# Kernel optimization log

Measured on AMD Instinct MI355X. Metric: run time of the kernel, lower is better.

Reference implementation:

```python
import jax, jax.numpy as jnp
import numpy as np

DEG_CLAMP = 1e6  # matches .clamp(max=1000000.0) on deg^-0.5


def setup_inputs() -> dict:
    key = jax.random.key(0)
    k1, k2, k3 = jax.random.split(key, 3)
    N, E, D_IN, D_OUT = 100000, 1600000, 128, 128
    x = jax.random.normal(k1, (N, D_IN), dtype=jnp.float32)
    edge_index = jax.random.randint(k2, (2, E), 0, N, dtype=jnp.int64)
    # Linear params (xavier_uniform on weight, zero-ish bias)
    limit = float(np.sqrt(6.0 / (D_IN + D_OUT)))
    W = jax.random.uniform(k3, (D_OUT, D_IN), dtype=jnp.float32, minval=-limit, maxval=limit)
    b = jnp.zeros((D_OUT,), dtype=jnp.float32)
    return {"x": x, "edge_index": edge_index, "W": W, "b": b}


def reference(x, edge_index, W, b):
    N = x.shape[0]
    # append self-loops: ei = cat([edge_index, [arange(N); arange(N)]], dim=1)
    self_idx = jnp.arange(N, dtype=edge_index.dtype)
    src = jnp.concatenate([edge_index[0], self_idx])  # [E+N]
    dst = jnp.concatenate([edge_index[1], self_idx])  # [E+N]
    # degree of destination nodes (with self-loops)
    deg = jax.ops.segment_sum(jnp.ones_like(dst, dtype=x.dtype), dst, num_segments=N)
    deg_inv_sqrt = jnp.minimum(deg ** -0.5, DEG_CLAMP)
    # linear transform (dropout is identity in eval)
    h = x @ W.T + b  # [N, D_OUT]
    # symmetric normalization, gather, scale, scatter-add
    norm = deg_inv_sqrt[src] * deg_inv_sqrt[dst]  # [E+N]
    msgs = h[src] * norm[:, None]                  # [E+N, D_OUT]
    out = jax.ops.segment_sum(msgs, dst, num_segments=N)  # [N, D_OUT]
    return out
```

## Files before the change

kernel.cpp:

```cpp
#include <hip/hip_runtime.h>
#include <hip/hip_bf16.h>
#include <cstddef>

#define D 128
#define SHIFT 9
#define RN (1 << SHIFT)
#define CAPLOG 14
#define CAP (1 << CAPLOG)

typedef __attribute__((ext_vector_type(8))) short bf16x8;
typedef __attribute__((ext_vector_type(16))) float f32x16;
typedef __attribute__((ext_vector_type(4))) float f32x4;

static __device__ __forceinline__ unsigned short f2bf(float f) {
  return __builtin_bit_cast(unsigned short, __float2bfloat16(f));
}
static __device__ __forceinline__ float bflo(unsigned u) {
  return __uint_as_float(u << 16);
}
static __device__ __forceinline__ float bfhi(unsigned u) {
  return __uint_as_float(u & 0xffff0000u);
}

__global__ void k_init(int* __restrict__ gcursor, int nc, unsigned* __restrict__ gz,
                       const float* __restrict__ W, unsigned short* __restrict__ Wbf) {
  const int t = blockIdx.x * 256 + threadIdx.x;
  if (t < nc) gcursor[t] = t << CAPLOG;
  if (t < 64) gz[t] = 0;
  if (t < 128 * 128) Wbf[t] = f2bf(W[t]);
}

__global__ __launch_bounds__(256) void k_psort(
    const int* __restrict__ src, const int* __restrict__ dst,
    int* __restrict__ gcursor, unsigned* __restrict__ pairs, int e, int nc) {
  __shared__ int hist4[4][256];
  const int tid = threadIdx.x;
  const int w = tid >> 6;
  const int base = blockIdx.x * 4096;
  const int m = min(4096, e - base);
#pragma unroll
  for (int u = 0; u < 4; ++u) ((int*)hist4)[tid + 256 * u] = 0;
  __syncthreads();
  int myd[16], mys[16];
#pragma unroll
  for (int j = 0; j < 16; ++j) {
    const int i = tid + j * 256;
    if (i < m) {
      myd[j] = dst[base + i];
      mys[j] = src[base + i];
      atomicAdd(&hist4[w][myd[j] >> SHIFT], 1);
    }
  }
  __syncthreads();
  if (tid < nc) {
    const int t0 = hist4[0][tid], t1 = hist4[1][tid];
    const int t2 = hist4[2][tid], t3 = hist4[3][tid];
    const int tot = t0 + t1 + t2 + t3;
    int b = (tot > 0) ? atomicAdd(&gcursor[tid], tot) : 0;
    hist4[0][tid] = b;
    hist4[1][tid] = b + t0;
    hist4[2][tid] = b + t0 + t1;
    hist4[3][tid] = b + t0 + t1 + t2;
  }
  __syncthreads();
#pragma unroll
  for (int j = 0; j < 16; ++j) {
    const int i = tid + j * 256;
    if (i < m) {
      const int c = myd[j] >> SHIFT;
      const int pos = atomicAdd(&hist4[w][c], 1);
      const unsigned pk = (unsigned)mys[j] | ((unsigned)(myd[j] & (RN - 1)) << 22);
      __builtin_nontemporal_store(pk, &pairs[pos]);
    }
  }
}

__global__ __launch_bounds__(512) void k_fine(
    const unsigned* __restrict__ pairs, const int* __restrict__ gcursor,
    int* __restrict__ rowptr, int* __restrict__ cnt, float* __restrict__ dinv,
    int* __restrict__ srcs, int n) {
  __shared__ int hist[RN];
  __shared__ int rowL[RN];
  __shared__ int sdata[RN];
  const int c = blockIdx.x;
  const int tid = threadIdx.x;
  const int node0 = c << SHIFT;
  const int nodes = min(RN, n - node0);
  hist[tid] = 0;
  __syncthreads();
  const int beg = c << CAPLOG;
  const int end = gcursor[c];
  for (int i = beg + tid; i < end; i += RN)
    atomicAdd(&hist[pairs[i] >> 22], 1);
  __syncthreads();
  const int deg = hist[tid];
  const int p = (deg + 15) & ~15;
  sdata[tid] = p;
  __syncthreads();
  for (int off = 1; off < RN; off <<= 1) {
    int t = (tid >= off) ? sdata[tid - off] : 0;
    __syncthreads();
    sdata[tid] += t;
    __syncthreads();
  }
  const int rbase = beg + sdata[tid] - p;
  rowL[tid] = rbase;
  hist[tid] = rbase;
  if (tid < nodes) {
    rowptr[node0 + tid] = rbase;
    cnt[node0 + tid] = p;
    dinv[node0 + tid] = fminf(rsqrtf((float)(deg + 1)), 1.0e6f);
  }
  __syncthreads();
  for (int i = beg + tid; i < end; i += RN) {
    const unsigned pr = pairs[i];
    const int pos = atomicAdd(&hist[pr >> 22], 1);
    srcs[pos] = (int)(pr & 0x3FFFFFu);
  }
  __syncthreads();
  const int fend = rowL[tid] + p;
  for (int i = hist[tid]; i < fend; ++i) srcs[i] = n;
}

__global__ __launch_bounds__(256) void k_gemm(
    const float* __restrict__ x, const unsigned short* __restrict__ Wbf,
    const float* __restrict__ bias, const float* __restrict__ dinv,
    __hip_bfloat16* __restrict__ g, int n) {
  __shared__ unsigned short xs[128 * 128];
  __shared__ unsigned short Ws[128 * 128];
  const int tid = threadIdx.x;
  const int row0 = blockIdx.x * 128;

#pragma unroll
  for (int u = 0; u < 8; ++u) {
    const int f = tid + 256 * u;
    const int row = f >> 4;
    const int c = f & 15;
    const int ch = (c ^ (row & 7)) << 3;
    *reinterpret_cast<uint4*>(&Ws[row * 128 + ch]) =
        *reinterpret_cast<const uint4*>(&Wbf[row * 128 + c * 8]);
    float4 v0 = make_float4(0.f, 0.f, 0.f, 0.f), v1 = v0;
    if (row0 + row < n) {
      const float4* p =
          reinterpret_cast<const float4*>(&x[(size_t)(row0 + row) * D + c * 8]);
      v0 = p[0]; v1 = p[1];
    }
    uint4 pk;
    pk.x = f2bf(v0.x) | ((unsigned)f2bf(v0.y) << 16);
    pk.y = f2bf(v0.z) | ((unsigned)f2bf(v0.w) << 16);
    pk.z = f2bf(v1.x) | ((unsigned)f2bf(v1.y) << 16);
    pk.w = f2bf(v1.z) | ((unsigned)f2bf(v1.w) << 16);
    *reinterpret_cast<uint4*>(&xs[row * 128 + ch]) = pk;
  }
  __syncthreads();

  const int lane = tid & 63;
  const int wv = tid >> 6;
  const int xr0 = (wv >> 1) * 64;
  const int cc0 = (wv & 1) * 64;
  const int lr = lane & 31;
  const int lk = lane >> 5;

  f32x16 acc[2][2];
#pragma unroll
  for (int p = 0; p < 2; ++p)
#pragma unroll
    for (int q = 0; q < 2; ++q)
#pragma unroll
      for (int t = 0; t < 16; ++t) acc[p][q][t] = 0.f;

#pragma unroll
  for (int ks = 0; ks < 8; ++ks) {
    bf16x8 a[2], b[2];
#pragma unroll
    for (int p = 0; p < 2; ++p) {
      const int r = cc0 + p * 32 + lr;
      const int ch = ((ks * 2 + lk) ^ (r & 7)) << 3;
      a[p] = *reinterpret_cast<const bf16x8*>(&Ws[r * 128 + ch]);
    }
#pragma unroll
    for (int q = 0; q < 2; ++q) {
      const int r = xr0 + q * 32 + lr;
      const int ch = ((ks * 2 + lk) ^ (r & 7)) << 3;
      b[q] = *reinterpret_cast<const bf16x8*>(&xs[r * 128 + ch]);
    }
#pragma unroll
    for (int p = 0; p < 2; ++p)
#pragma unroll
      for (int q = 0; q < 2; ++q)
        acc[p][q] = __builtin_amdgcn_mfma_f32_32x32x16_bf16(a[p], b[q], acc[p][q], 0, 0, 0);
  }

#pragma unroll
  for (int q = 0; q < 2; ++q) {
    const int r = row0 + xr0 + q * 32 + lr;
    if (r < n) {
      const float dv = dinv[r];
#pragma unroll
      for (int p = 0; p < 2; ++p) {
#pragma unroll
        for (int rg = 0; rg < 4; ++rg) {
          const int cb = cc0 + p * 32 + 8 * rg + 4 * lk;
          const float v0 = (acc[p][q][rg * 4 + 0] + bias[cb + 0]) * dv;
          const float v1 = (acc[p][q][rg * 4 + 1] + bias[cb + 1]) * dv;
          const float v2 = (acc[p][q][rg * 4 + 2] + bias[cb + 2]) * dv;
          const float v3 = (acc[p][q][rg * 4 + 3] + bias[cb + 3]) * dv;
          uint2 pk;
          pk.x = f2bf(v0) | ((unsigned)f2bf(v1) << 16);
          pk.y = f2bf(v2) | ((unsigned)f2bf(v3) << 16);
          *reinterpret_cast<uint2*>(&g[(size_t)r * D + cb]) = pk;
        }
      }
    }
  }
}

__global__ __launch_bounds__(256) void k_accum(
    const int* __restrict__ rowptr, const int* __restrict__ cnt,
    const int* __restrict__ srcs, const uint2* __restrict__ gq,
    const float* __restrict__ dinv, float* __restrict__ out, int n) {
  const int w = (int)(((size_t)blockIdx.x * 256 + threadIdx.x) >> 6);
  const int lane = threadIdx.x & 63;
  if (w >= n) return;
  const int li = lane & 31;
  const int half = lane >> 5;
  const int beg = rowptr[w];
  const int num = cnt[w];

  const uint2 sv = gq[(size_t)(half ? n : w) * 32 + li];
  float a0 = bflo(sv.x), a1 = bfhi(sv.x), a2 = bflo(sv.y), a3 = bfhi(sv.y);

  if (num > 0) {
    const int4* s4 = (const int4*)(srcs + beg);
    int4 q0 = s4[0], q1 = s4[1], q2 = s4[2], q3 = s4[3];
    for (int k = 0; k < num; k += 16) {
      const int nx = (k + 16 < num) ? ((k + 16) >> 2) : 0;
      const int4 n0 = s4[nx], n1 = s4[nx + 1], n2 = s4[nx + 2], n3 = s4[nx + 3];
      const int e0 = half ? q0.y : q0.x, e1 = half ? q0.w : q0.z;
      const int e2 = half ? q1.y : q1.x, e3 = half ? q1.w : q1.z;
      const int e4 = half ? q2.y : q2.x, e5 = half ? q2.w : q2.z;
      const int e6 = half ? q3.y : q3.x, e7 = half ? q3.w : q3.z;
      const uint2 t0 = gq[(size_t)e0 * 32 + li];
      const uint2 t1 = gq[(size_t)e1 * 32 + li];
      const uint2 t2 = gq[(size_t)e2 * 32 + li];
      const uint2 t3 = gq[(size_t)e3 * 32 + li];
      const uint2 t4 = gq[(size_t)e4 * 32 + li];
      const uint2 t5 = gq[(size_t)e5 * 32 + li];
      const uint2 t6 = gq[(size_t)e6 * 32 + li];
      const uint2 t7 = gq[(size_t)e7 * 32 + li];
      a0 += bflo(t0.x) + bflo(t1.x) + bflo(t2.x) + bflo(t3.x) +
            bflo(t4.x) + bflo(t5.x) + bflo(t6.x) + bflo(t7.x);
      a1 += bfhi(t0.x) + bfhi(t1.x) + bfhi(t2.x) + bfhi(t3.x) +
            bfhi(t4.x) + bfhi(t5.x) + bfhi(t6.x) + bfhi(t7.x);
      a2 += bflo(t0.y) + bflo(t1.y) + bflo(t2.y) + bflo(t3.y) +
            bflo(t4.y) + bflo(t5.y) + bflo(t6.y) + bflo(t7.y);
      a3 += bfhi(t0.y) + bfhi(t1.y) + bfhi(t2.y) + bfhi(t3.y) +
            bfhi(t4.y) + bfhi(t5.y) + bfhi(t6.y) + bfhi(t7.y);
      q0 = n0; q1 = n1; q2 = n2; q3 = n3;
    }
  }

  a0 += __shfl_xor(a0, 32);
  a1 += __shfl_xor(a1, 32);
  a2 += __shfl_xor(a2, 32);
  a3 += __shfl_xor(a3, 32);

  if (!half) {
    const float dv = dinv[w];
    f32x4 res;
    res[0] = a0 * dv; res[1] = a1 * dv; res[2] = a2 * dv; res[3] = a3 * dv;
    f32x4* dst = (f32x4*)(out + (size_t)w * D) + li;
    __builtin_nontemporal_store(res, dst);
  }
}

extern "C" void kernel_launch(void* const* d_in, const int* in_sizes, int n_in,
                              void* d_out, int out_size, void* d_ws, size_t ws_size,
                              hipStream_t stream) {
  const float* x = (const float*)d_in[0];
  const int* ei = (const int*)d_in[1];
  const float* W = (const float*)d_in[2];
  const float* b = (const float*)d_in[3];
  float* out = (float*)d_out;
  const int n = in_sizes[0] / D;
  const int e = in_sizes[1] / 2;
  const int* src = ei;
  const int* dst = ei + e;
  const int nc = (n + RN - 1) >> SHIFT;

  char* ws = (char*)d_ws;
  const size_t nbb = ((size_t)n * 4 + 255) / 256 * 256;
  const size_t pb = (((size_t)nc << CAPLOG) * 4 + 255) / 256 * 256;
  float* dinv = (float*)ws;
  int* rowptr = (int*)(ws + nbb);
  int* cnt = (int*)(ws + 2 * nbb);
  int* gcursor = (int*)(ws + 3 * nbb);
  unsigned short* Wbf = (unsigned short*)(ws + 3 * nbb + 1024);
  int* srcs = (int*)(ws + 3 * nbb + 1024 + 32768);
  char* pr_base = ws + 3 * nbb + 1024 + 32768 + pb;
  unsigned* pairs = (unsigned*)pr_base;
  __hip_bfloat16* g = (__hip_bfloat16*)pr_base;

  k_init<<<64, 256, 0, stream>>>(gcursor, nc, (unsigned*)(g + (size_t)n * D), W, Wbf);
  k_psort<<<(e + 4095) / 4096, 256, 0, stream>>>(src, dst, gcursor, pairs, e, nc);
  k_fine<<<nc, RN, 0, stream>>>(pairs, gcursor, rowptr, cnt, dinv, srcs, n);
  k_gemm<<<(n + 127) / 128, 256, 0, stream>>>(x, Wbf, b, dinv, g, n);
  k_accum<<<(n + 3) / 4, 256, 0, stream>>>(rowptr, cnt, srcs, (const uint2*)g,
                                           dinv, out, n);
}
```

Baseline: 176.1 us.

## Use nontemporal and vectorized loads; keep W fragments in registers for GEMM

Edge-index loads in the partition sort become 128-bit vector nontemporal loads, with an explicit -1 sentinel marking invalid slots. The pairs, x and srcs streams are read with nontemporal hints so single-use data does not pollute the cache. The GEMM drops the shared-memory copy of W and loads each wave's W fragments straight into registers, which halves LDS use and removes LDS reads. The cost is higher register pressure in the GEMM, and the vector path assumes the edge index arrays are 16-byte aligned.

```diff
diff --git a/kernel.cpp b/kernel.cpp
--- a/kernel.cpp
+++ b/kernel.cpp
@@ -11,6 +11,7 @@
 typedef __attribute__((ext_vector_type(8))) short bf16x8;
 typedef __attribute__((ext_vector_type(16))) float f32x16;
 typedef __attribute__((ext_vector_type(4))) float f32x4;
+typedef __attribute__((ext_vector_type(4))) int i32x4;
 
 static __device__ __forceinline__ unsigned short f2bf(float f) {
   return __builtin_bit_cast(unsigned short, __float2bfloat16(f));
@@ -43,12 +44,31 @@
   __syncthreads();
   int myd[16], mys[16];
 #pragma unroll
-  for (int j = 0; j < 16; ++j) {
-    const int i = tid + j * 256;
-    if (i < m) {
-      myd[j] = dst[base + i];
-      mys[j] = src[base + i];
-      atomicAdd(&hist4[w][myd[j] >> SHIFT], 1);
+  for (int j = 0; j < 4; ++j) {
+    const int i4 = tid + j * 256;
+    const int i = i4 * 4;
+    if (i + 3 < m) {
+      const i32x4 d4 = __builtin_nontemporal_load(
+          reinterpret_cast<const i32x4*>(dst + base) + i4);
+      const i32x4 s4 = __builtin_nontemporal_load(
+          reinterpret_cast<const i32x4*>(src + base) + i4);
+#pragma unroll
+      for (int u = 0; u < 4; ++u) {
+        myd[j * 4 + u] = d4[u]; mys[j * 4 + u] = s4[u];
+        atomicAdd(&hist4[w][d4[u] >> SHIFT], 1);
+      }
+    } else {
+#pragma unroll
+      for (int u = 0; u < 4; ++u) {
+        const int ii = i + u;
+        if (ii < m) {
+          myd[j * 4 + u] = dst[base + ii];
+          mys[j * 4 + u] = src[base + ii];
+          atomicAdd(&hist4[w][myd[j * 4 + u] >> SHIFT], 1);
+        } else {
+          myd[j * 4 + u] = -1;
+        }
+      }
     }
   }
   __syncthreads();
@@ -65,8 +85,7 @@
   __syncthreads();
 #pragma unroll
   for (int j = 0; j < 16; ++j) {
-    const int i = tid + j * 256;
-    if (i < m) {
+    if (myd[j] >= 0) {
       const int c = myd[j] >> SHIFT;
       const int pos = atomicAdd(&hist4[w][c], 1);
       const unsigned pk = (unsigned)mys[j] | ((unsigned)(myd[j] & (RN - 1)) << 22);
@@ -91,7 +110,7 @@
   const int beg = c << CAPLOG;
   const int end = gcursor[c];
   for (int i = beg + tid; i < end; i += RN)
-    atomicAdd(&hist[pairs[i] >> 22], 1);
+    atomicAdd(&hist[__builtin_nontemporal_load(&pairs[i]) >> 22], 1);
   __syncthreads();
   const int deg = hist[tid];
   const int p = (deg + 15) & ~15;
@@ -113,7 +132,7 @@
   }
   __syncthreads();
   for (int i = beg + tid; i < end; i += RN) {
-    const unsigned pr = pairs[i];
+    const unsigned pr = __builtin_nontemporal_load(&pairs[i]);
     const int pos = atomicAdd(&hist[pr >> 22], 1);
     srcs[pos] = (int)(pr & 0x3FFFFFu);
   }
@@ -127,33 +146,8 @@
     const float* __restrict__ bias, const float* __restrict__ dinv,
     __hip_bfloat16* __restrict__ g, int n) {
   __shared__ unsigned short xs[128 * 128];
-  __shared__ unsigned short Ws[128 * 128];
   const int tid = threadIdx.x;
   const int row0 = blockIdx.x * 128;
-
-#pragma unroll
-  for (int u = 0; u < 8; ++u) {
-    const int f = tid + 256 * u;
-    const int row = f >> 4;
-    const int c = f & 15;
-    const int ch = (c ^ (row & 7)) << 3;
-    *reinterpret_cast<uint4*>(&Ws[row * 128 + ch]) =
-        *reinterpret_cast<const uint4*>(&Wbf[row * 128 + c * 8]);
-    float4 v0 = make_float4(0.f, 0.f, 0.f, 0.f), v1 = v0;
-    if (row0 + row < n) {
-      const float4* p =
-          reinterpret_cast<const float4*>(&x[(size_t)(row0 + row) * D + c * 8]);
-      v0 = p[0]; v1 = p[1];
-    }
-    uint4 pk;
-    pk.x = f2bf(v0.x) | ((unsigned)f2bf(v0.y) << 16);
-    pk.y = f2bf(v0.z) | ((unsigned)f2bf(v0.w) << 16);
-    pk.z = f2bf(v1.x) | ((unsigned)f2bf(v1.y) << 16);
-    pk.w = f2bf(v1.z) | ((unsigned)f2bf(v1.w) << 16);
-    *reinterpret_cast<uint4*>(&xs[row * 128 + ch]) = pk;
-  }
-  __syncthreads();
-
   const int lane = tid & 63;
   const int wv = tid >> 6;
   const int xr0 = (wv >> 1) * 64;
@@ -161,6 +155,36 @@
   const int lr = lane & 31;
   const int lk = lane >> 5;
 
+  bf16x8 Wf[2][8];
+#pragma unroll
+  for (int p = 0; p < 2; ++p) {
+    const int r = cc0 + p * 32 + lr;
+#pragma unroll
+    for (int ks = 0; ks < 8; ++ks)
+      Wf[p][ks] = *reinterpret_cast<const bf16x8*>(&Wbf[r * 128 + ks * 16 + lk * 8]);
+  }
+
+#pragma unroll
+  for (int u = 0; u < 8; ++u) {
+    const int f = tid + 256 * u;
+    const int row = f >> 4;
+    const int c = f & 15;
+    const int ch = (c ^ (row & 7)) << 3;
+    f32x4 v0 = {0.f, 0.f, 0.f, 0.f}, v1 = v0;
+    if (row0 + row < n) {
+      const f32x4* p = reinterpret_cast<const f32x4*>(&x[(size_t)(row0 + row) * D + c * 8]);
+      v0 = __builtin_nontemporal_load(p);
+      v1 = __builtin_nontemporal_load(p + 1);
+    }
+    uint4 pk;
+    pk.x = f2bf(v0[0]) | ((unsigned)f2bf(v0[1]) << 16);
+    pk.y = f2bf(v0[2]) | ((unsigned)f2bf(v0[3]) << 16);
+    pk.z = f2bf(v1[0]) | ((unsigned)f2bf(v1[1]) << 16);
+    pk.w = f2bf(v1[2]) | ((unsigned)f2bf(v1[3]) << 16);
+    *reinterpret_cast<uint4*>(&xs[row * 128 + ch]) = pk;
+  }
+  __syncthreads();
+
   f32x16 acc[2][2];
 #pragma unroll
   for (int p = 0; p < 2; ++p)
@@ -171,13 +195,7 @@
 
 #pragma unroll
   for (int ks = 0; ks < 8; ++ks) {
-    bf16x8 a[2], b[2];
-#pragma unroll
-    for (int p = 0; p < 2; ++p) {
-      const int r = cc0 + p * 32 + lr;
-      const int ch = ((ks * 2 + lk) ^ (r & 7)) << 3;
-      a[p] = *reinterpret_cast<const bf16x8*>(&Ws[r * 128 + ch]);
-    }
+    bf16x8 b[2];
 #pragma unroll
     for (int q = 0; q < 2; ++q) {
       const int r = xr0 + q * 32 + lr;
@@ -188,7 +206,7 @@
     for (int p = 0; p < 2; ++p)
 #pragma unroll
       for (int q = 0; q < 2; ++q)
-        acc[p][q] = __builtin_amdgcn_mfma_f32_32x32x16_bf16(a[p], b[q], acc[p][q], 0, 0, 0);
+        acc[p][q] = __builtin_amdgcn_mfma_f32_32x32x16_bf16(Wf[p][ks], b[q], acc[p][q], 0, 0, 0);
   }
 
 #pragma unroll
@@ -231,15 +249,21 @@
   float a0 = bflo(sv.x), a1 = bfhi(sv.x), a2 = bflo(sv.y), a3 = bfhi(sv.y);
 
   if (num > 0) {
-    const int4* s4 = (const int4*)(srcs + beg);
-    int4 q0 = s4[0], q1 = s4[1], q2 = s4[2], q3 = s4[3];
+    const i32x4* s4 = (const i32x4*)(srcs + beg);
+    i32x4 q0 = __builtin_nontemporal_load(s4);
+    i32x4 q1 = __builtin_nontemporal_load(s4 + 1);
+    i32x4 q2 = __builtin_nontemporal_load(s4 + 2);
+    i32x4 q3 = __builtin_nontemporal_load(s4 + 3);
     for (int k = 0; k < num; k += 16) {
       const int nx = (k + 16 < num) ? ((k + 16) >> 2) : 0;
-      const int4 n0 = s4[nx], n1 = s4[nx + 1], n2 = s4[nx + 2], n3 = s4[nx + 3];
-      const int e0 = half ? q0.y : q0.x, e1 = half ? q0.w : q0.z;
-      const int e2 = half ? q1.y : q1.x, e3 = half ? q1.w : q1.z;
-      const int e4 = half ? q2.y : q2.x, e5 = half ? q2.w : q2.z;
-      const int e6 = half ? q3.y : q3.x, e7 = half ? q3.w : q3.z;
+      const i32x4 n0 = __builtin_nontemporal_load(s4 + nx);
+      const i32x4 n1 = __builtin_nontemporal_load(s4 + nx + 1);
+      const i32x4 n2 = __builtin_nontemporal_load(s4 + nx + 2);
+      const i32x4 n3 = __builtin_nontemporal_load(s4 + nx + 3);
+      const int e0 = half ? q0[1] : q0[0], e1 = half ? q0[3] : q0[2];
+      const int e2 = half ? q1[1] : q1[0], e3 = half ? q1[3] : q1[2];
+      const int e4 = half ? q2[1] : q2[0], e5 = half ? q2[3] : q2[2];
+      const int e6 = half ? q3[1] : q3[0], e7 = half ? q3[3] : q3[2];
       const uint2 t0 = gq[(size_t)e0 * 32 + li];
       const uint2 t1 = gq[(size_t)e1 * 32 + li];
       const uint2 t2 = gq[(size_t)e2 * 32 + li];
```

Measured after the change: 190.3 us. 1.08x slower.
